# Optimization experiments

Measured on AMD Instinct MI355X. Metric: run time of the kernel, lower is better.

Reference implementation:

```python
import jax, jax.numpy as jnp
import numpy as np
import math

D_MODEL = 1024
HEADS = 16
HEAD_DIM = D_MODEL // HEADS
BATCH = 2
SEQ = 2048


def setup_inputs() -> dict:
    key = jax.random.key(0)
    ks = jax.random.split(key, 6)
    scale = 1.0 / math.sqrt(D_MODEL)
    return {
        "x": jax.random.normal(ks[0], (BATCH, SEQ, D_MODEL), dtype=jnp.float32),
        "mask": jnp.zeros((SEQ, SEQ), dtype=jnp.float32),
        "w_qkv": jax.random.normal(ks[1], (D_MODEL, 3 * D_MODEL), dtype=jnp.float32) * scale,
        "b_qkv": jax.random.normal(ks[2], (3 * D_MODEL,), dtype=jnp.float32) * 0.01,
        "w_out": jax.random.normal(ks[3], (D_MODEL, D_MODEL), dtype=jnp.float32) * scale,
        "b_out": jax.random.normal(ks[4], (D_MODEL,), dtype=jnp.float32) * 0.01,
    }


def reference(x, mask, w_qkv, b_qkv, w_out, b_out):
    B, S, D = x.shape
    H, hd = HEADS, HEAD_DIM
    # fused QKV projection: [B,S,3D]
    qkv = x @ w_qkv + b_qkv
    # [B,S,H,3*hd] -> [B,H,S,3*hd]
    qkv = qkv.reshape(B, S, H, 3 * hd).transpose(0, 2, 1, 3)
    q, k, v = jnp.split(qkv, 3, axis=-1)  # each [B,H,S,hd]
    inv_sqrt_d = jnp.asarray(1.0 / math.sqrt(hd), dtype=x.dtype)
    scores = jnp.einsum("bhqd,bhkd->bhqk", q, k) * inv_sqrt_d
    # additive mask; [S,S] broadcasts identically in [H,B,S,S] or [B,H,S,S] layout
    scores = scores + mask
    attn = jax.nn.softmax(scores, axis=-1)
    vals = jnp.einsum("bhqk,bhkd->bhqd", attn, v)  # [B,H,S,hd]
    vals = vals.transpose(0, 2, 1, 3).reshape(B, S, H * hd)
    return vals @ w_out + b_out
```

## Files before the change

### kernel.cpp

```cpp
#include <hip/hip_runtime.h>


typedef __bf16 bf16;
typedef __bf16 bf16x2 __attribute__((ext_vector_type(2)));
typedef __bf16 bf16x4 __attribute__((ext_vector_type(4)));
typedef __bf16 bf16x8 __attribute__((ext_vector_type(8)));
typedef float f32x4 __attribute__((ext_vector_type(4)));

#define MFMA(a, b, c) __builtin_amdgcn_mfma_f32_16x16x32_bf16((a), (b), (c), 0, 0, 0)

#if __has_builtin(__builtin_amdgcn_exp2f)
#define EXP2(x) __builtin_amdgcn_exp2f(x)
#else
#define EXP2(x) exp2f(x)
#endif

__device__ __forceinline__ void load_lds16(const bf16* g, void* l) {
    __builtin_amdgcn_global_load_lds(
        (const __attribute__((address_space(1))) unsigned int*)g,
        (__attribute__((address_space(3))) unsigned int*)l, 16, 0, 0);
}

__global__ void cast4_kernel(const float* __restrict__ in, bf16* __restrict__ out, int n4) {
    int i = blockIdx.x * blockDim.x + threadIdx.x;
    if (i < n4) {
        float4 v = ((const float4*)in)[i];
        bf16x4 o = {(bf16)v.x, (bf16)v.y, (bf16)v.z, (bf16)v.w};
        ((bf16x4*)out)[i] = o;
    }
}

__global__ void transpose_cast_kernel(const float* __restrict__ in, bf16* __restrict__ out,
                                      int R, int C) {
    __shared__ float tile[32][33];
    int bx = blockIdx.x * 32;
    int by = blockIdx.y * 32;
    int tx = threadIdx.x, ty = threadIdx.y;
    for (int i = 0; i < 32; i += 8)
        tile[ty + i][tx] = in[(size_t)(by + ty + i) * C + bx + tx];
    __syncthreads();
    for (int i = 0; i < 32; i += 8)
        out[(size_t)(bx + ty + i) * R + by + tx] = (bf16)tile[tx][ty + i];
}

__global__ __launch_bounds__(256) void gemm_qkv_kernel(
    const bf16* __restrict__ A, const bf16* __restrict__ BT,
    const float* __restrict__ bias,
    bf16* __restrict__ Q, bf16* __restrict__ K, bf16* __restrict__ VT) {
    __shared__ __attribute__((aligned(16))) char lds[4][16384];
    int bm = blockIdx.x, bn = blockIdx.y;
    int t = threadIdx.x;
    int w = t >> 6, lane = t & 63, g = lane >> 4, l16 = lane & 15;
    int wm = (w >> 1) * 64, wn = (w & 1) * 64;
    f32x4 acc[4][4] = {};
    const bf16* Ablk = A + (size_t)(bm * 128) * 1024;
    const bf16* Bblk = BT + (size_t)(bn * 128) * 1024;
    int srow = t >> 2;
    int scg = (t & 3) ^ (srow & 3);
    const bf16* ag0 = Ablk + (size_t)srow * 1024 + scg * 8;
    const bf16* ag1 = ag0 + 64 * 1024;
    const bf16* bg0 = Bblk + (size_t)srow * 1024 + scg * 8;
    const bf16* bg1 = bg0 + 64 * 1024;

    load_lds16(ag0, lds[0] + t * 16);
    load_lds16(ag1, lds[0] + 4096 + t * 16);
    load_lds16(bg0, lds[0] + 8192 + t * 16);
    load_lds16(bg1, lds[0] + 12288 + t * 16);
    load_lds16(ag0 + 32, lds[1] + t * 16);
    load_lds16(ag1 + 32, lds[1] + 4096 + t * 16);
    load_lds16(bg0 + 32, lds[1] + 8192 + t * 16);
    load_lds16(bg1 + 32, lds[1] + 12288 + t * 16);
    asm volatile("s_waitcnt vmcnt(0)" ::: "memory");
    asm volatile("s_barrier" ::: "memory");

    int sw = l16 & 3;
#pragma unroll 4
    for (int j = 0; j < 32; j++) {
        int buf = j & 3;
        int jp = j + 2 < 32 ? j + 2 : 31;
        char* dst = lds[(j + 2) & 3];
        load_lds16(ag0 + jp * 32, dst + t * 16);
        load_lds16(ag1 + jp * 32, dst + 4096 + t * 16);
        load_lds16(bg0 + jp * 32, dst + 8192 + t * 16);
        load_lds16(bg1 + jp * 32, dst + 12288 + t * 16);
        asm volatile("s_waitcnt vmcnt(8)" ::: "memory");
        asm volatile("s_barrier" ::: "memory");

        const bf16* As = (const bf16*)lds[buf];
        const bf16* Bs = (const bf16*)(lds[buf] + 8192);
        bf16x8 af[4], bfr[4];
#pragma unroll
        for (int mi = 0; mi < 4; mi++) {
            int row = wm + mi * 16 + l16;
            af[mi] = *(const bf16x8*)(&As[row * 32 + (g ^ sw) * 8]);
        }
#pragma unroll
        for (int ni = 0; ni < 4; ni++) {
            int row = wn + ni * 16 + l16;
            bfr[ni] = *(const bf16x8*)(&Bs[row * 32 + (g ^ sw) * 8]);
        }
#pragma unroll
        for (int mi = 0; mi < 4; mi++)
#pragma unroll
            for (int ni = 0; ni < 4; ni++)
                acc[mi][ni] = MFMA(af[mi], bfr[ni], acc[mi][ni]);
    }
    asm volatile("s_waitcnt vmcnt(0)" ::: "memory");

    for (int mi = 0; mi < 4; mi++) {
        int row0 = bm * 128 + wm + mi * 16 + g * 4;
        int b = row0 >> 11, s0 = row0 & 2047;
        for (int ni = 0; ni < 4; ni++) {
            int col = bn * 128 + wn + ni * 16 + l16;
            float bv = bias[col];
            int h = col / 192, tt = col % 192;
            size_t bh = (size_t)(b * 16 + h);
            if (tt < 128) {
                bf16* dst = (tt < 64) ? &Q[(bh * 2048 + s0) * 64 + tt]
                                      : &K[(bh * 2048 + s0) * 64 + (tt - 64)];
                for (int r = 0; r < 4; r++)
                    dst[(size_t)r * 64] = (bf16)(acc[mi][ni][r] + bv);
            } else {
                bf16x4 pk = {(bf16)(acc[mi][ni][0] + bv), (bf16)(acc[mi][ni][1] + bv),
                             (bf16)(acc[mi][ni][2] + bv), (bf16)(acc[mi][ni][3] + bv)};
                *(bf16x4*)(&VT[(bh * 64 + (tt - 128)) * 2048 + s0]) = pk;
            }
        }
    }
}

__global__ __launch_bounds__(256) void gemm_out_kernel(
    const bf16* __restrict__ A, const bf16* __restrict__ BT,
    const float* __restrict__ bias, float* __restrict__ out) {
    __shared__ __attribute__((aligned(16))) char lds[4][12288];
    int bm = blockIdx.x, bn = blockIdx.y;
    int t = threadIdx.x;
    int w = t >> 6, lane = t & 63, g = lane >> 4, l16 = lane & 15;
    int wm = (w >> 1) * 64, wn = (w & 1) * 32;
    f32x4 acc[4][2] = {};
    const bf16* Ablk = A + (size_t)(bm * 128) * 1024;
    const bf16* Bblk = BT + (size_t)(bn * 64) * 1024;
    int srow = t >> 2;
    int scg = (t & 3) ^ (srow & 3);
    const bf16* ag0 = Ablk + (size_t)srow * 1024 + scg * 8;
    const bf16* ag1 = ag0 + 64 * 1024;
    const bf16* bg0 = Bblk + (size_t)srow * 1024 + scg * 8;

    load_lds16(ag0, lds[0] + t * 16);
    load_lds16(ag1, lds[0] + 4096 + t * 16);
    load_lds16(bg0, lds[0] + 8192 + t * 16);
    load_lds16(ag0 + 32, lds[1] + t * 16);
    load_lds16(ag1 + 32, lds[1] + 4096 + t * 16);
    load_lds16(bg0 + 32, lds[1] + 8192 + t * 16);
    asm volatile("s_waitcnt vmcnt(0)" ::: "memory");
    asm volatile("s_barrier" ::: "memory");

    int sw = l16 & 3;
#pragma unroll 4
    for (int j = 0; j < 32; j++) {
        int buf = j & 3;
        int jp = j + 2 < 32 ? j + 2 : 31;
        char* dst = lds[(j + 2) & 3];
        load_lds16(ag0 + jp * 32, dst + t * 16);
        load_lds16(ag1 + jp * 32, dst + 4096 + t * 16);
        load_lds16(bg0 + jp * 32, dst + 8192 + t * 16);
        asm volatile("s_waitcnt vmcnt(6)" ::: "memory");
        asm volatile("s_barrier" ::: "memory");

        const bf16* As = (const bf16*)lds[buf];
        const bf16* Bs = (const bf16*)(lds[buf] + 8192);
        bf16x8 af[4], bfr[2];
#pragma unroll
        for (int mi = 0; mi < 4; mi++) {
            int row = wm + mi * 16 + l16;
            af[mi] = *(const bf16x8*)(&As[row * 32 + (g ^ sw) * 8]);
        }
#pragma unroll
        for (int ni = 0; ni < 2; ni++) {
            int row = wn + ni * 16 + l16;
            bfr[ni] = *(const bf16x8*)(&Bs[row * 32 + (g ^ sw) * 8]);
        }
#pragma unroll
        for (int mi = 0; mi < 4; mi++)
#pragma unroll
            for (int ni = 0; ni < 2; ni++)
                acc[mi][ni] = MFMA(af[mi], bfr[ni], acc[mi][ni]);
    }
    asm volatile("s_waitcnt vmcnt(0)" ::: "memory");

    for (int mi = 0; mi < 4; mi++) {
        for (int ni = 0; ni < 2; ni++) {
            int col = bn * 64 + wn + ni * 16 + l16;
            float bv = bias[col];
            for (int r = 0; r < 4; r++) {
                int row = bm * 128 + wm + mi * 16 + g * 4 + r;
                out[(size_t)row * 1024 + col] = acc[mi][ni][r] + bv;
            }
        }
    }
}

__global__ __launch_bounds__(256, 4) void attn_kernel(
    const bf16* __restrict__ Q, const bf16* __restrict__ K,
    const bf16* __restrict__ VT, const float* __restrict__ mask,
    bf16* __restrict__ vals) {
    __shared__ __attribute__((aligned(16))) char lds[4][8192];

    int blk = blockIdx.x;
    int bh = ((blk & 7) << 2) | ((blk >> 3) & 3);
    int qt = blk >> 5;
    int t = threadIdx.x;
    int w = t >> 6, lane = t & 63, g = lane >> 4, l16 = lane & 15;
    int qw = qt * 64 + w * 16;

    const bf16* Qp = Q + (size_t)bh * 2048 * 64;
    const bf16* Kp = K + (size_t)bh * 2048 * 64;
    const bf16* Vp = VT + (size_t)bh * 64 * 2048;
    const float* mrow = mask + (size_t)(qw + l16) * 2048;

    int ks_row = t >> 3;
    int ks_cblk = (t & 7) ^ (ks_row & 7);
    const bf16* kg = Kp + ks_row * 64 + ks_cblk * 8;
    int vs_d = t >> 2;
    int vs_sblk = (t & 3) ^ ((t >> 3) & 3);
    const bf16* vg = Vp + (size_t)vs_d * 2048 + vs_sblk * 8;

    const float SCL = 0.125f * 1.44269504089f;
    const float L2E = 1.44269504089f;

    bf16x8 q0 = *(const bf16x8*)(&Qp[(size_t)(qw + l16) * 64 + g * 8]);
    bf16x8 q1 = *(const bf16x8*)(&Qp[(size_t)(qw + l16) * 64 + 32 + g * 8]);
    load_lds16(kg + 0, &lds[0][t * 16]);
    load_lds16(vg + 0, &lds[0][4096 + t * 16]);
    float4 mv0 = *(const float4*)(&mrow[0 + g * 4]);
    float4 mv1 = *(const float4*)(&mrow[16 + g * 4]);
    load_lds16(kg + 1 * 32 * 64, &lds[1][t * 16]);
    load_lds16(vg + 1 * 32, &lds[1][4096 + t * 16]);
    asm volatile("s_waitcnt vmcnt(0)" ::: "memory");
    asm volatile("s_barrier" ::: "memory");

    f32x4 o[4] = {};
    float m = -1e30f, l = 0.f;

#pragma unroll 4
    for (int j = 0; j < 64; j++) {
        int buf = j & 3;
        int jm = j + 1 < 64 ? j + 1 : 63;
        float4 nmv0 = *(const float4*)(&mrow[jm * 32 + g * 4]);
        float4 nmv1 = *(const float4*)(&mrow[jm * 32 + 16 + g * 4]);
        int jp = j + 2 < 64 ? j + 2 : 63;
        load_lds16(kg + (size_t)jp * 32 * 64, &lds[(j + 2) & 3][t * 16]);
        load_lds16(vg + jp * 32, &lds[(j + 2) & 3][4096 + t * 16]);
        asm volatile("s_waitcnt vmcnt(8)" ::: "memory");
        asm volatile("s_barrier" ::: "memory");

        float sc[8];
#pragma unroll
        for (int ts = 0; ts < 2; ts++) {
            int s0 = ts * 16 + l16;
            int sw = s0 & 7;
            bf16x8 k0 = *(const bf16x8*)(&lds[buf][(s0 * 8 + (g ^ sw)) * 16]);
            bf16x8 k1 = *(const bf16x8*)(&lds[buf][(s0 * 8 + ((4 + g) ^ sw)) * 16]);
            f32x4 st = {};
            st = MFMA(k0, q0, st);
            st = MFMA(k1, q1, st);
            float4 mv = ts ? *(float4*)&mv1 : *(float4*)&mv0;
            sc[ts * 4 + 0] = st[0] * SCL + mv.x * L2E;
            sc[ts * 4 + 1] = st[1] * SCL + mv.y * L2E;
            sc[ts * 4 + 2] = st[2] * SCL + mv.z * L2E;
            sc[ts * 4 + 3] = st[3] * SCL + mv.w * L2E;
        }

        float vmax = sc[0];
#pragma unroll
        for (int i = 1; i < 8; i++) vmax = fmaxf(vmax, sc[i]);
        vmax = fmaxf(vmax, __shfl_xor(vmax, 16, 64));
        vmax = fmaxf(vmax, __shfl_xor(vmax, 32, 64));
        float mold = m;
        float mn = fmaxf(mold, vmax);
        m = mn;
        float p[8], rs = 0.f;
#pragma unroll
        for (int i = 0; i < 8; i++) { p[i] = EXP2(sc[i] - mn); rs += p[i]; }
        rs += __shfl_xor(rs, 16, 64);
        rs += __shfl_xor(rs, 32, 64);
        if (__any(vmax > mold)) {
            float alpha = EXP2(mold - mn);
            l = l * alpha + rs;
#pragma unroll
            for (int nc = 0; nc < 4; nc++) {
                o[nc][0] *= alpha; o[nc][1] *= alpha;
                o[nc][2] *= alpha; o[nc][3] *= alpha;
            }
        } else {
            l += rs;
        }

        int dw0, dw1, dw2, dw3;
        { union { bf16x2 h; int i; } u;
          u.h = bf16x2{(bf16)p[0], (bf16)p[1]}; dw0 = u.i;
          u.h = bf16x2{(bf16)p[2], (bf16)p[3]}; dw1 = u.i;
          u.h = bf16x2{(bf16)p[4], (bf16)p[5]}; dw2 = u.i;
          u.h = bf16x2{(bf16)p[6], (bf16)p[7]}; dw3 = u.i; }
        int selA = (((2 * g) & 3) << 4) | l16;
        int selB = (((2 * g + 1) & 3) << 4) | l16;
        int t0a = __shfl(dw0, selA, 64), t2a = __shfl(dw2, selA, 64);
        int t1a = __shfl(dw1, selA, 64), t3a = __shfl(dw3, selA, 64);
        int t0b = __shfl(dw0, selB, 64), t2b = __shfl(dw2, selB, 64);
        int t1b = __shfl(dw1, selB, 64), t3b = __shfl(dw3, selB, 64);
        bool hi = (g & 2) != 0;
        union { int i[4]; bf16x8 v; } pu;
        pu.i[0] = hi ? t2a : t0a;
        pu.i[1] = hi ? t3a : t1a;
        pu.i[2] = hi ? t2b : t0b;
        pu.i[3] = hi ? t3b : t1b;

#pragma unroll
        for (int nc = 0; nc < 4; nc++) {
            int d = nc * 16 + l16;
            int slot = d * 4 + (g ^ ((d >> 1) & 3));
            bf16x8 vf = *(const bf16x8*)(&lds[buf][4096 + slot * 16]);
            o[nc] = MFMA(vf, pu.v, o[nc]);
        }

        mv0 = nmv0;
        mv1 = nmv1;
    }
    asm volatile("s_waitcnt vmcnt(0)" ::: "memory");

    int b = bh >> 4, h = bh & 15;
    float linv = 1.f / l;
    size_t row = (size_t)(b * 2048 + qw + l16);
#pragma unroll
    for (int nc = 0; nc < 4; nc++) {
        bf16x4 pk = {(bf16)(o[nc][0] * linv), (bf16)(o[nc][1] * linv),
                     (bf16)(o[nc][2] * linv), (bf16)(o[nc][3] * linv)};
        *(bf16x4*)(&vals[row * 1024 + h * 64 + nc * 16 + g * 4]) = pk;
    }
}

extern "C" void kernel_launch(void* const* d_in, const int* in_sizes, int n_in,
                              void* d_out, int out_size, void* d_ws, size_t ws_size,
                              hipStream_t stream) {
    const float* x     = (const float*)d_in[0];
    const float* mask  = (const float*)d_in[1];
    const float* w_qkv = (const float*)d_in[2];
    const float* b_qkv = (const float*)d_in[3];
    const float* w_out = (const float*)d_in[4];
    const float* b_out = (const float*)d_in[5];
    float* out = (float*)d_out;

    char* ws = (char*)d_ws;
    size_t off = 0;
    bf16* xb    = (bf16*)(ws + off); off += (size_t)4096 * 1024 * 2;
    bf16* wqkvT = (bf16*)(ws + off); off += (size_t)3072 * 1024 * 2;
    bf16* woutT = (bf16*)(ws + off); off += (size_t)1024 * 1024 * 2;
    bf16* Qa    = (bf16*)(ws + off); off += (size_t)32 * 2048 * 64 * 2;
    bf16* Ka    = (bf16*)(ws + off); off += (size_t)32 * 2048 * 64 * 2;
    bf16* VTa   = (bf16*)(ws + off); off += (size_t)32 * 64 * 2048 * 2;
    bf16* vals  = (bf16*)(ws + off); off += (size_t)4096 * 1024 * 2;

    cast4_kernel<<<4096, 256, 0, stream>>>(x, xb, 4096 * 1024 / 4);
    transpose_cast_kernel<<<dim3(96, 32), dim3(32, 8), 0, stream>>>(w_qkv, wqkvT, 1024, 3072);
    transpose_cast_kernel<<<dim3(32, 32), dim3(32, 8), 0, stream>>>(w_out, woutT, 1024, 1024);
    gemm_qkv_kernel<<<dim3(32, 24), 256, 0, stream>>>(xb, wqkvT, b_qkv, Qa, Ka, VTa);
    attn_kernel<<<1024, 256, 0, stream>>>(Qa, Ka, VTa, mask, vals);
    gemm_out_kernel<<<dim3(32, 16), 256, 0, stream>>>(vals, woutT, b_out, out);
}
```

Before: 240.9 us.

## Simplify GEMM pipelines to double buffering and make softmax rescale unconditional

```diff
diff --git a/kernel.cpp b/kernel.cpp
--- a/kernel.cpp
+++ b/kernel.cpp
@@ -47,7 +47,7 @@
     const bf16* __restrict__ A, const bf16* __restrict__ BT,
     const float* __restrict__ bias,
     bf16* __restrict__ Q, bf16* __restrict__ K, bf16* __restrict__ VT) {
-    __shared__ __attribute__((aligned(16))) char lds[4][16384];
+    __shared__ __attribute__((aligned(16))) char lds[2][16384];
     int bm = blockIdx.x, bn = blockIdx.y;
     int t = threadIdx.x;
     int w = t >> 6, lane = t & 63, g = lane >> 4, l16 = lane & 15;
@@ -66,28 +66,21 @@
     load_lds16(ag1, lds[0] + 4096 + t * 16);
     load_lds16(bg0, lds[0] + 8192 + t * 16);
     load_lds16(bg1, lds[0] + 12288 + t * 16);
-    load_lds16(ag0 + 32, lds[1] + t * 16);
-    load_lds16(ag1 + 32, lds[1] + 4096 + t * 16);
-    load_lds16(bg0 + 32, lds[1] + 8192 + t * 16);
-    load_lds16(bg1 + 32, lds[1] + 12288 + t * 16);
     asm volatile("s_waitcnt vmcnt(0)" ::: "memory");
-    asm volatile("s_barrier" ::: "memory");
 
     int sw = l16 & 3;
-#pragma unroll 4
+#pragma unroll 2
     for (int j = 0; j < 32; j++) {
-        int buf = j & 3;
-        int jp = j + 2 < 32 ? j + 2 : 31;
-        char* dst = lds[(j + 2) & 3];
+        asm volatile("s_barrier" ::: "memory");
+        int jp = j + 1 < 32 ? j + 1 : 31;
+        char* dst = lds[(j + 1) & 1];
         load_lds16(ag0 + jp * 32, dst + t * 16);
         load_lds16(ag1 + jp * 32, dst + 4096 + t * 16);
         load_lds16(bg0 + jp * 32, dst + 8192 + t * 16);
         load_lds16(bg1 + jp * 32, dst + 12288 + t * 16);
-        asm volatile("s_waitcnt vmcnt(8)" ::: "memory");
-        asm volatile("s_barrier" ::: "memory");
-
-        const bf16* As = (const bf16*)lds[buf];
-        const bf16* Bs = (const bf16*)(lds[buf] + 8192);
+
+        const bf16* As = (const bf16*)lds[j & 1];
+        const bf16* Bs = (const bf16*)(lds[j & 1] + 8192);
         bf16x8 af[4], bfr[4];
 #pragma unroll
         for (int mi = 0; mi < 4; mi++) {
@@ -104,8 +97,8 @@
 #pragma unroll
             for (int ni = 0; ni < 4; ni++)
                 acc[mi][ni] = MFMA(af[mi], bfr[ni], acc[mi][ni]);
-    }
-    asm volatile("s_waitcnt vmcnt(0)" ::: "memory");
+        asm volatile("s_waitcnt vmcnt(0)" ::: "memory");
+    }
 
     for (int mi = 0; mi < 4; mi++) {
         int row0 = bm * 128 + wm + mi * 16 + g * 4;
@@ -132,7 +125,7 @@
 __global__ __launch_bounds__(256) void gemm_out_kernel(
     const bf16* __restrict__ A, const bf16* __restrict__ BT,
     const float* __restrict__ bias, float* __restrict__ out) {
-    __shared__ __attribute__((aligned(16))) char lds[4][12288];
+    __shared__ __attribute__((aligned(16))) char lds[2][12288];
     int bm = blockIdx.x, bn = blockIdx.y;
     int t = threadIdx.x;
     int w = t >> 6, lane = t & 63, g = lane >> 4, l16 = lane & 15;
@@ -149,26 +142,20 @@
     load_lds16(ag0, lds[0] + t * 16);
     load_lds16(ag1, lds[0] + 4096 + t * 16);
     load_lds16(bg0, lds[0] + 8192 + t * 16);
-    load_lds16(ag0 + 32, lds[1] + t * 16);
-    load_lds16(ag1 + 32, lds[1] + 4096 + t * 16);
-    load_lds16(bg0 + 32, lds[1] + 8192 + t * 16);
     asm volatile("s_waitcnt vmcnt(0)" ::: "memory");
-    asm volatile("s_barrier" ::: "memory");
 
     int sw = l16 & 3;
-#pragma unroll 4
+#pragma unroll 2
     for (int j = 0; j < 32; j++) {
-        int buf = j & 3;
-        int jp = j + 2 < 32 ? j + 2 : 31;
-        char* dst = lds[(j + 2) & 3];
+        asm volatile("s_barrier" ::: "memory");
+        int jp = j + 1 < 32 ? j + 1 : 31;
+        char* dst = lds[(j + 1) & 1];
         load_lds16(ag0 + jp * 32, dst + t * 16);
         load_lds16(ag1 + jp * 32, dst + 4096 + t * 16);
         load_lds16(bg0 + jp * 32, dst + 8192 + t * 16);
-        asm volatile("s_waitcnt vmcnt(6)" ::: "memory");
-        asm volatile("s_barrier" ::: "memory");
-
-        const bf16* As = (const bf16*)lds[buf];
-        const bf16* Bs = (const bf16*)(lds[buf] + 8192);
+
+        const bf16* As = (const bf16*)lds[j & 1];
+        const bf16* Bs = (const bf16*)(lds[j & 1] + 8192);
         bf16x8 af[4], bfr[2];
 #pragma unroll
         for (int mi = 0; mi < 4; mi++) {
@@ -185,8 +172,8 @@
 #pragma unroll
             for (int ni = 0; ni < 2; ni++)
                 acc[mi][ni] = MFMA(af[mi], bfr[ni], acc[mi][ni]);
-    }
-    asm volatile("s_waitcnt vmcnt(0)" ::: "memory");
+        asm volatile("s_waitcnt vmcnt(0)" ::: "memory");
+    }
 
     for (int mi = 0; mi < 4; mi++) {
         for (int ni = 0; ni < 2; ni++) {
@@ -242,7 +229,6 @@
     f32x4 o[4] = {};
     float m = -1e30f, l = 0.f;
 
-#pragma unroll 4
     for (int j = 0; j < 64; j++) {
         int buf = j & 3;
         int jm = j + 1 < 64 ? j + 1 : 63;
@@ -276,24 +262,18 @@
         for (int i = 1; i < 8; i++) vmax = fmaxf(vmax, sc[i]);
         vmax = fmaxf(vmax, __shfl_xor(vmax, 16, 64));
         vmax = fmaxf(vmax, __shfl_xor(vmax, 32, 64));
-        float mold = m;
-        float mn = fmaxf(mold, vmax);
+        float mn = fmaxf(m, vmax);
+        float alpha = EXP2(m - mn);
         m = mn;
         float p[8], rs = 0.f;
 #pragma unroll
         for (int i = 0; i < 8; i++) { p[i] = EXP2(sc[i] - mn); rs += p[i]; }
         rs += __shfl_xor(rs, 16, 64);
         rs += __shfl_xor(rs, 32, 64);
-        if (__any(vmax > mold)) {
-            float alpha = EXP2(mold - mn);
-            l = l * alpha + rs;
-#pragma unroll
-            for (int nc = 0; nc < 4; nc++) {
-                o[nc][0] *= alpha; o[nc][1] *= alpha;
-                o[nc][2] *= alpha; o[nc][3] *= alpha;
-            }
-        } else {
-            l += rs;
+        l = l * alpha + rs;
+#pragma unroll
+        for (int nc = 0; nc < 4; nc++) {
+            o[nc][0] *= alpha; o[nc][1] *= alpha; o[nc][2] *= alpha; o[nc][3] *= alpha;
         }
 
         int dw0, dw1, dw2, dw3;
```

New measurement: 241.9 us. Within noise of the previous version (+0.4%).
